# Kernel optimization log

Measured on AMD Instinct MI355X. Metric: run time of the kernel, lower is better.

Reference implementation:

```python
import jax, jax.numpy as jnp
import numpy as np

B, S, T = 4, 512, 512
V, D, F, H, DK, N = 32000, 512, 2048, 8, 64, 6
PAD = 0

# sinusoidal positional encoding table, matching the torch source exactly
_pos = np.arange(max(S, T))[:, None]
_i = np.arange(D // 2)[None, :]
_ang = _pos / (10000.0 ** (2 * _i / D))
_pe = np.empty((max(S, T), D), dtype=np.float32)
_pe[:, 0::2] = np.sin(_ang)
_pe[:, 1::2] = np.cos(_ang)
PE = jnp.asarray(_pe)


def setup_inputs() -> dict:
    key = jax.random.key(0)
    ks = iter(jax.random.split(key, 64))
    s = 0.02
    w = lambda shape: jax.random.normal(next(ks), shape, jnp.float32) * s
    inp = {
        'src': jax.random.randint(next(ks), (B, S), 0, V, jnp.int32),
        'trg': jax.random.randint(next(ks), (B, T), 0, V, jnp.int32),
        'emb_src': w((V, D)).at[PAD].set(0.0),
        'emb_trg': w((V, D)).at[PAD].set(0.0),
        # encoder stacks (leading axis = layer)
        'enc_wq': w((N, D, H * DK)), 'enc_wk': w((N, D, H * DK)),
        'enc_wv': w((N, D, H * DK)), 'enc_wo': w((N, H * DK, D)),
        'enc_ln1_g': jnp.ones((N, D)), 'enc_ln1_b': jnp.zeros((N, D)),
        'enc_w1': w((N, D, F)), 'enc_b1': jnp.zeros((N, F)),
        'enc_w2': w((N, F, D)), 'enc_b2': jnp.zeros((N, D)),
        'enc_ln2_g': jnp.ones((N, D)), 'enc_ln2_b': jnp.zeros((N, D)),
        # decoder stacks
        'dec_wq': w((N, D, H * DK)), 'dec_wk': w((N, D, H * DK)),
        'dec_wv': w((N, D, H * DK)), 'dec_wo': w((N, H * DK, D)),
        'dec_ln1_g': jnp.ones((N, D)), 'dec_ln1_b': jnp.zeros((N, D)),
        'dec_cq': w((N, D, H * DK)), 'dec_ck': w((N, D, H * DK)),
        'dec_cv': w((N, D, H * DK)), 'dec_co': w((N, H * DK, D)),
        'dec_ln2_g': jnp.ones((N, D)), 'dec_ln2_b': jnp.zeros((N, D)),
        'dec_w1': w((N, D, F)), 'dec_b1': jnp.zeros((N, F)),
        'dec_w2': w((N, F, D)), 'dec_b2': jnp.zeros((N, D)),
        'dec_ln3_g': jnp.ones((N, D)), 'dec_ln3_b': jnp.zeros((N, D)),
        'proj': w((D, V)),
    }
    return inp


def _ln(x, g, b, eps=1e-5):
    m = x.mean(-1, keepdims=True)
    v = ((x - m) ** 2).mean(-1, keepdims=True)
    return (x - m) * jax.lax.rsqrt(v + eps) * g + b


def _mha(xq, xkv, wq, wk, wv, wo, mask):
    b, lq, _ = xq.shape
    lk = xkv.shape[1]
    q = (xq @ wq).reshape(b, lq, H, DK).transpose(0, 2, 1, 3)   # bhqd
    k = (xkv @ wk).reshape(b, lk, H, DK).transpose(0, 2, 1, 3)  # bhkd
    v = (xkv @ wv).reshape(b, lk, H, DK).transpose(0, 2, 1, 3)  # bhkd
    scores = jnp.einsum('bhqd,bhkd->bhqk', q, k)
    scores = jnp.where(mask, -jnp.inf, scores)
    attn = jax.nn.softmax(scores * (DK ** -0.5), axis=-1)
    out = jnp.einsum('bhqk,bhkd->bhqd', attn, v)
    out = out.transpose(0, 2, 1, 3).reshape(b, lq, H * DK)
    return out @ wo


def _ffn(x, w1, b1, w2, b2):
    return jax.nn.relu(x @ w1 + b1) @ w2 + b2


def reference(src, trg, emb_src, emb_trg,
              enc_wq, enc_wk, enc_wv, enc_wo, enc_ln1_g, enc_ln1_b,
              enc_w1, enc_b1, enc_w2, enc_b2, enc_ln2_g, enc_ln2_b,
              dec_wq, dec_wk, dec_wv, dec_wo, dec_ln1_g, dec_ln1_b,
              dec_cq, dec_ck, dec_cv, dec_co, dec_ln2_g, dec_ln2_b,
              dec_w1, dec_b1, dec_w2, dec_b2, dec_ln3_g, dec_ln3_b,
              proj):
    scale = D ** 0.5
    src_pad = (src == PAD)[:, None, None, :]                 # [B,1,1,S]
    trg_pad = (trg == PAD)[:, None, None, :]                 # [B,1,1,T]
    causal = jnp.triu(jnp.ones((T, T), bool), 1)[None, None]  # [1,1,T,T]
    trg_mask = trg_pad | causal

    # encoder (dropout = identity in eval)
    x = emb_src[src] * scale + PE[None, :S]

    def enc_step(h, p):
        wq, wk, wv, wo, g1, b1, w1, bb1, w2, bb2, g2, b2 = p
        h = _ln(h + _mha(h, h, wq, wk, wv, wo, src_pad), g1, b1)
        h = _ln(h + _ffn(h, w1, bb1, w2, bb2), g2, b2)
        return h, None

    x_enc, _ = jax.lax.scan(enc_step, x,
        (enc_wq, enc_wk, enc_wv, enc_wo, enc_ln1_g, enc_ln1_b,
         enc_w1, enc_b1, enc_w2, enc_b2, enc_ln2_g, enc_ln2_b))

    # decoder
    y = emb_trg[trg] * scale + PE[None, :T]

    def dec_step(h, p):
        (wq, wk, wv, wo, g1, b1, cq, ck, cv, co, g2, b2,
         w1, bb1, w2, bb2, g3, b3) = p
        h = _ln(h + _mha(h, h, wq, wk, wv, wo, trg_mask), g1, b1)
        h = _ln(h + _mha(h, x_enc, cq, ck, cv, co, src_pad), g2, b2)
        h = _ln(h + _ffn(h, w1, bb1, w2, bb2), g3, b3)
        return h, None

    y, _ = jax.lax.scan(dec_step, y,
        (dec_wq, dec_wk, dec_wv, dec_wo, dec_ln1_g, dec_ln1_b,
         dec_cq, dec_ck, dec_cv, dec_co, dec_ln2_g, dec_ln2_b,
         dec_w1, dec_b1, dec_w2, dec_b2, dec_ln3_g, dec_ln3_b))

    return y @ proj  # [B, T, trg_vocab]
```

## Files before the change

kernel.cpp:

```cpp
#include <hip/hip_runtime.h>
#include <math.h>

#define BBATCH 4
#define SS 512
#define DDIM 512
#define FFN 2048
#define NHEAD 8
#define DHEAD 64
#define NL 6
#define NVOC 32000
#define MTOK (BBATCH*SS)
#define PAD_ID 0
#define MSZE ((size_t)MTOK * DDIM)

typedef unsigned short u16;
typedef __attribute__((ext_vector_type(8))) short short8;
typedef __attribute__((ext_vector_type(4))) float f32x4;

__device__ __forceinline__ u16 f2bf(float f) {
    union { float f; unsigned u; } v; v.f = f;
    unsigned r = ((v.u >> 16) & 1u) + 0x7fffu;
    return (u16)((v.u + r) >> 16);
}

__device__ __forceinline__ void gload16(const u16* g, u16* l) {
    __builtin_amdgcn_global_load_lds(
        (const __attribute__((address_space(1))) void*)g,
        (__attribute__((address_space(3))) void*)l, 16, 0, 0);
}

template<int N> __device__ __forceinline__ void waitv() {
    if constexpr (N == 0)      asm volatile("s_waitcnt vmcnt(0)" ::: "memory");
    else if constexpr (N == 2) asm volatile("s_waitcnt vmcnt(2)" ::: "memory");
    else if constexpr (N == 3) asm volatile("s_waitcnt vmcnt(3)" ::: "memory");
    else if constexpr (N == 4) asm volatile("s_waitcnt vmcnt(4)" ::: "memory");
    else if constexpr (N == 6) asm volatile("s_waitcnt vmcnt(6)" ::: "memory");
    else if constexpr (N == 8) asm volatile("s_waitcnt vmcnt(8)" ::: "memory");
    __builtin_amdgcn_sched_barrier(0);
}
__device__ __forceinline__ void rawbar() {
    __builtin_amdgcn_s_barrier();
    __builtin_amdgcn_sched_barrier(0);
}

template<int BM, int BN, int OUTBF, int RELU, int BIAS>
__device__ __forceinline__ void gemm_core(
    u16* __restrict__ AsB, u16* __restrict__ BsB,
    const u16* __restrict__ A, int lda,
    const u16* __restrict__ B, int ldb,
    void* __restrict__ Cv, int ldc,
    int row0, int col0, int K, const float* __restrict__ bias)
{
    const int tid  = threadIdx.x;
    const int lane = tid & 63;
    const int wid  = tid >> 6;
    const int wr   = wid >> 1, wc = wid & 1;
    constexpr int MF = BM / 32, NF = BN / 32, RA = BM / 64, RB = BN / 64;
    constexpr int LPT = RA + RB;

    const u16* aSrc[RA]; int aOff[RA];
    #pragma unroll
    for (int r = 0; r < RA; r++) {
        int row = (tid >> 2) + r * 64;
        int slot = ((tid & 3) << 4) ^ ((row & 3) << 4);
        aSrc[r] = A + (size_t)(row0 + row) * lda + (slot >> 1);
        aOff[r] = r * 2048 + tid * 8;
    }
    const u16* bSrc[RB]; int bOff[RB];
    #pragma unroll
    for (int r = 0; r < RB; r++) {
        int row = (tid >> 2) + r * 64;
        int slot = ((tid & 3) << 4) ^ ((row & 3) << 4);
        bSrc[r] = B + (size_t)(col0 + row) * ldb + (slot >> 1);
        bOff[r] = r * 2048 + tid * 8;
    }

    f32x4 acc[MF][NF];
    const f32x4 zero = {0.f, 0.f, 0.f, 0.f};
    #pragma unroll
    for (int m = 0; m < MF; m++)
        #pragma unroll
        for (int n = 0; n < NF; n++) acc[m][n] = zero;

    auto issue = [&](int t) {
        u16* ad = AsB + (t & 3) * (BM * 32);
        u16* bd = BsB + (t & 3) * (BN * 32);
        #pragma unroll
        for (int r = 0; r < RA; r++) gload16(aSrc[r] + t * 32, ad + aOff[r]);
        #pragma unroll
        for (int r = 0; r < RB; r++) gload16(bSrc[r] + t * 32, bd + bOff[r]);
    };
    auto comp = [&](int t) {
        const u16* as = AsB + (t & 3) * (BM * 32);
        const u16* bs = BsB + (t & 3) * (BN * 32);
        short8 af[MF], bf[NF];
        #pragma unroll
        for (int m = 0; m < MF; m++) {
            int row = wr * (BM / 2) + m * 16 + (lane & 15);
            int slot = ((lane >> 4) << 4) ^ ((row & 3) << 4);
            af[m] = *(const short8*)&as[row * 32 + (slot >> 1)];
        }
        #pragma unroll
        for (int n = 0; n < NF; n++) {
            int row = wc * (BN / 2) + n * 16 + (lane & 15);
            int slot = ((lane >> 4) << 4) ^ ((row & 3) << 4);
            bf[n] = *(const short8*)&bs[row * 32 + (slot >> 1)];
        }
        __builtin_amdgcn_s_setprio(1);
        #pragma unroll
        for (int m = 0; m < MF; m++)
            #pragma unroll
            for (int n = 0; n < NF; n++)
                acc[m][n] = __builtin_amdgcn_mfma_f32_16x16x32_bf16(af[m], bf[n], acc[m][n], 0, 0, 0);
        __builtin_amdgcn_s_setprio(0);
    };

    const int nt = K / 32;
    issue(0); issue(1); issue(2);
    int t = 0;
    for (; t < nt - 2; ++t) {
        waitv<2 * LPT>();
        rawbar();
        if (t + 3 < nt) issue(t + 3);
        comp(t);
    }
    waitv<LPT>(); rawbar(); comp(nt - 2);
    waitv<0>();   rawbar(); comp(nt - 1);

    const int crow = row0 + wr * (BM / 2);
    const int ccol = col0 + wc * (BN / 2);
    #pragma unroll
    for (int m = 0; m < MF; m++) {
        #pragma unroll
        for (int n = 0; n < NF; n++) {
            int col = ccol + n * 16 + (lane & 15);
            float bv = BIAS ? bias[col] : 0.0f;
            #pragma unroll
            for (int i = 0; i < 4; i++) {
                int row = crow + m * 16 + ((lane >> 4) << 2) + i;
                float v = acc[m][n][i] + bv;
                if (RELU) v = fmaxf(v, 0.0f);
                if (OUTBF) ((u16*)Cv)[(size_t)row * ldc + col] = f2bf(v);
                else       ((float*)Cv)[(size_t)row * ldc + col] = v;
            }
        }
    }
}

template<int BM, int BN, int OUTBF, int RELU, int BIAS, int SWZ = 0>
__global__ __launch_bounds__(256) void mgemm(
    const u16* __restrict__ A, int lda, size_t aSb, size_t aSh,
    const u16* __restrict__ B, int ldb, size_t bSb, size_t bSh,
    void* __restrict__ Cv, int ldc, size_t cSb, size_t cSh,
    int K, const float* __restrict__ bias)
{
    __shared__ __align__(16) u16 As[4 * BM * 32];
    __shared__ __align__(16) u16 Bs[4 * BN * 32];
    int bx = blockIdx.x, by = blockIdx.y;
    if (SWZ) {
        int nwg = gridDim.x * gridDim.y;
        int lin = by * gridDim.x + bx;
        int cpx = nwg >> 3;
        int s = (lin & 7) * cpx + (lin >> 3);
        bx = s % gridDim.x; by = s / gridDim.x;
    }
    const int zb = blockIdx.z >> 3, zh = blockIdx.z & 7;
    const u16* Ab = A + (size_t)zb * aSb + (size_t)zh * aSh;
    const u16* Bb = B + (size_t)zb * bSb + (size_t)zh * bSh;
    void* Cb = OUTBF ? (void*)((u16*)Cv + (size_t)zb * cSb + (size_t)zh * cSh)
                     : (void*)((float*)Cv + (size_t)zb * cSb + (size_t)zh * cSh);
    gemm_core<BM, BN, OUTBF, RELU, BIAS>(As, Bs, Ab, lda, Bb, ldb, Cb, ldc,
                                          by * BM, bx * BN, K, bias);
}

template<int BM, int BN>
__global__ __launch_bounds__(256) void mgemm_dual(
    const u16* __restrict__ A1, int lda1, const u16* __restrict__ B1, int ldb1,
    u16* __restrict__ C1, int ldc1, int nx1, int nblk1,
    const u16* __restrict__ A2, int lda2, const u16* __restrict__ B2, int ldb2,
    u16* __restrict__ C2, int ldc2, int nx2,
    int K)
{
    __shared__ __align__(16) u16 As[4 * BM * 32];
    __shared__ __align__(16) u16 Bs[4 * BN * 32];
    int id = blockIdx.x;
    if (id < nblk1) {
        gemm_core<BM, BN, 1, 0, 0>(As, Bs, A1, lda1, B1, ldb1, C1, ldc1,
                                    (id / nx1) * BM, (id % nx1) * BN, K, nullptr);
    } else {
        id -= nblk1;
        gemm_core<BM, BN, 1, 0, 0>(As, Bs, A2, lda2, B2, ldb2, C2, ldc2,
                                    (id / nx2) * BM, (id % nx2) * BN, K, nullptr);
    }
}

template<int CAUSAL>
__global__ __launch_bounds__(512) void flash_attn(
    const u16* __restrict__ Qp, int ldq,
    const u16* __restrict__ Kp, int ldk,
    const u16* __restrict__ Vtp,
    u16* __restrict__ O,
    const int* __restrict__ ids)
{
    __shared__ __align__(16) u16 Kl[3][64 * 64];
    __shared__ __align__(16) u16 Vl[3][64 * 64];
    __shared__ __align__(16) u16 Pl[8][16 * 64];
    __shared__ float msk[SS];

    const int tid = threadIdx.x, lane = tid & 63, wid = tid >> 6;
    const int bh = blockIdx.y, b = bh >> 3, h = bh & 7;
    const int q0 = blockIdx.x * 128;

    for (int i = tid; i < SS; i += 512)
        msk[i] = (ids[b * SS + i] == PAD_ID) ? -1e30f : 0.0f;

    const int qloc = wid * 16 + (lane & 15);
    const u16* Qb = Qp + (size_t)(b * SS + q0 + qloc) * ldq + h * 64 + ((lane >> 4) * 8);
    short8 qf[2];
    qf[0] = *(const short8*)(Qb);
    qf[1] = *(const short8*)(Qb + 32);

    const u16* Kb = Kp + (size_t)b * SS * ldk + h * 64;
    const u16* Vb = Vtp + (size_t)(h * 64) * MTOK + b * SS;

    auto stage = [&](int buf, int kt) {
        int row = tid >> 3;
        int sl  = tid & 7;
        int ls = sl ^ (row & 7);
        gload16(Kb + (size_t)(kt * 64 + row) * ldk + ls * 8, &Kl[buf][row * 64 + sl * 8]);
        gload16(Vb + (size_t)row * MTOK + kt * 64 + ls * 8, &Vl[buf][row * 64 + sl * 8]);
    };

    const int nt = CAUSAL ? (2 * blockIdx.x + 2) : (SS / 64);

    float m_i[4], l_i[4];
    f32x4 o_acc[4];
    const f32x4 zero = {0.f, 0.f, 0.f, 0.f};
    #pragma unroll
    for (int i = 0; i < 4; i++) { m_i[i] = -1e30f; l_i[i] = 0.0f; }
    #pragma unroll
    for (int n = 0; n < 4; n++) o_acc[n] = zero;

    auto comp = [&](int kt) {
        const int cur = kt % 3;
        f32x4 s_acc[4];
        #pragma unroll
        for (int n = 0; n < 4; n++) s_acc[n] = zero;
        __builtin_amdgcn_s_setprio(1);
        #pragma unroll
        for (int kk = 0; kk < 2; kk++) {
            #pragma unroll
            for (int n = 0; n < 4; n++) {
                int row = n * 16 + (lane & 15);
                int ls = (kk * 4 + (lane >> 4)) ^ (row & 7);
                short8 kf = *(const short8*)&Kl[cur][row * 64 + ls * 8];
                s_acc[n] = __builtin_amdgcn_mfma_f32_16x16x32_bf16(qf[kk], kf, s_acc[n], 0, 0, 0);
            }
        }
        __builtin_amdgcn_s_setprio(0);

        float sv[4][4];
        #pragma unroll
        for (int n = 0; n < 4; n++) {
            int kg = kt * 64 + n * 16 + (lane & 15);
            float mk = msk[kg];
            #pragma unroll
            for (int i = 0; i < 4; i++) {
                float s = s_acc[n][i] * 0.125f + mk;
                if (CAUSAL) {
                    int qg = q0 + wid * 16 + ((lane >> 4) << 2) + i;
                    if (kg > qg) s = -1e30f;
                }
                sv[n][i] = s;
            }
        }
        float pm[4], mn[4], rs[4], ps[4];
        #pragma unroll
        for (int i = 0; i < 4; i++)
            pm[i] = fmaxf(fmaxf(sv[0][i], sv[1][i]), fmaxf(sv[2][i], sv[3][i]));
        #pragma unroll
        for (int i = 0; i < 4; i++) {
            #pragma unroll
            for (int msh = 1; msh <= 8; msh <<= 1)
                pm[i] = fmaxf(pm[i], __shfl_xor(pm[i], msh));
            mn[i] = fmaxf(m_i[i], pm[i]);
            rs[i] = __expf(m_i[i] - mn[i]);
            m_i[i] = mn[i];
        }
        float p[4][4];
        #pragma unroll
        for (int n = 0; n < 4; n++)
            #pragma unroll
            for (int i = 0; i < 4; i++)
                p[n][i] = (sv[n][i] < -1e29f) ? 0.0f : __expf(sv[n][i] - mn[i]);
        #pragma unroll
        for (int i = 0; i < 4; i++) {
            ps[i] = p[0][i] + p[1][i] + p[2][i] + p[3][i];
            #pragma unroll
            for (int msh = 1; msh <= 8; msh <<= 1)
                ps[i] += __shfl_xor(ps[i], msh);
            l_i[i] = l_i[i] * rs[i] + ps[i];
        }
        #pragma unroll
        for (int n = 0; n < 4; n++)
            #pragma unroll
            for (int i = 0; i < 4; i++)
                o_acc[n][i] *= rs[i];

        #pragma unroll
        for (int n = 0; n < 4; n++) {
            int k = n * 16 + (lane & 15);
            #pragma unroll
            for (int i = 0; i < 4; i++) {
                int q = ((lane >> 4) << 2) + i;
                Pl[wid][q * 64 + (((k >> 3) ^ (q & 7)) << 3) + (k & 7)] = f2bf(p[n][i]);
            }
        }
        asm volatile("s_waitcnt lgkmcnt(0)" ::: "memory");
        __builtin_amdgcn_sched_barrier(0);

        __builtin_amdgcn_s_setprio(1);
        #pragma unroll
        for (int kk = 0; kk < 2; kk++) {
            int qrow = lane & 15;
            int lsp = (kk * 4 + (lane >> 4)) ^ (qrow & 7);
            short8 pa = *(const short8*)&Pl[wid][qrow * 64 + lsp * 8];
            #pragma unroll
            for (int nf = 0; nf < 4; nf++) {
                int row = nf * 16 + (lane & 15);
                int vs = (kk * 4 + (lane >> 4)) ^ (row & 7);
                short8 vf = *(const short8*)&Vl[cur][row * 64 + vs * 8];
                o_acc[nf] = __builtin_amdgcn_mfma_f32_16x16x32_bf16(pa, vf, o_acc[nf], 0, 0, 0);
            }
        }
        __builtin_amdgcn_s_setprio(0);
    };

    stage(0, 0);
    stage(1, 1);
    int t = 0;
    for (; t < nt - 1; ++t) {
        waitv<2>();
        rawbar();
        if (t + 2 < nt) stage((t + 2) % 3, t + 2);
        comp(t);
    }
    waitv<0>(); rawbar(); comp(nt - 1);

    #pragma unroll
    for (int nf = 0; nf < 4; nf++) {
        int d = h * 64 + nf * 16 + (lane & 15);
        #pragma unroll
        for (int i = 0; i < 4; i++) {
            int qg = b * SS + q0 + wid * 16 + ((lane >> 4) << 2) + i;
            O[(size_t)qg * DDIM + d] = f2bf(o_acc[nf][i] / l_i[i]);
        }
    }
}

__device__ __forceinline__ void transp_core(const float* __restrict__ src, u16* __restrict__ dst,
                                            int N, int K, int n0, int k0)
{
    __shared__ u16 t[64][65];
    const int tid = threadIdx.x;
    #pragma unroll
    for (int i = 0; i < 16; i++) {
        int idx = tid + i * 256;
        int kr = idx >> 6, nc = idx & 63;
        t[kr][nc] = f2bf(src[(size_t)(k0 + kr) * N + n0 + nc]);
    }
    __syncthreads();
    #pragma unroll
    for (int i = 0; i < 16; i++) {
        int idx = tid + i * 256;
        int nr = idx >> 6, kc = idx & 63;
        dst[(size_t)(n0 + nr) * K + k0 + kc] = t[kc][nr];
    }
}

__global__ __launch_bounds__(256) void transp(const float* __restrict__ src, u16* __restrict__ dst,
                                              int N, int K, size_t sStride, size_t dStride)
{
    transp_core(src + (size_t)blockIdx.z * sStride, dst + (size_t)blockIdx.z * dStride,
                N, K, blockIdx.x * 64, blockIdx.y * 64);
}

#define OFF_QK 0u
#define OFF_WV 524288u
#define OFF_WO 786432u
#define OFF_CQ 1048576u
#define OFF_CK 1310720u
#define OFF_CV 1572864u
#define OFF_CO 1835008u
#define OFF_W1 2097152u
#define OFF_W2 3145728u
#define WBLK   4194304u
#define M2CNT  262144u
#define MF1CNT 1048576u

__global__ __launch_bounds__(256) void transpW(
    const float* p0, const float* p1, const float* p2, const float* p3,
    const float* p4, const float* p5, const float* p6, const float* p7,
    const float* p8, const float* p9, const float* p10, const float* p11,
    u16* __restrict__ wreg)
{
    int z = blockIdx.z;
    int w = z % 12, l = z / 12;
    const float* ptrs[12] = {p0,p1,p2,p3,p4,p5,p6,p7,p8,p9,p10,p11};
    const float* src = ptrs[w] + (size_t)l * M2CNT;
    u16* dst = wreg + (w < 4 ? (size_t)l * WBLK + (size_t)w * M2CNT
                             : (size_t)(NL + l) * WBLK + (size_t)(w - 4) * M2CNT);
    transp_core(src, dst, 512, 512, blockIdx.x * 64, blockIdx.y * 64);
}

__global__ __launch_bounds__(256) void transpF1(const float* __restrict__ e,
                                                const float* __restrict__ d, u16* __restrict__ wreg)
{
    int z = blockIdx.z; int l = z % NL, w = z / NL;
    const float* src = (w ? d : e) + (size_t)l * MF1CNT;
    u16* dst = wreg + (size_t)(w * NL + l) * WBLK + OFF_W1;
    transp_core(src, dst, 2048, 512, blockIdx.x * 64, blockIdx.y * 64);
}

__global__ __launch_bounds__(256) void transpF2(const float* __restrict__ e,
                                                const float* __restrict__ d, u16* __restrict__ wreg)
{
    int z = blockIdx.z; int l = z % NL, w = z / NL;
    const float* src = (w ? d : e) + (size_t)l * MF1CNT;
    u16* dst = wreg + (size_t)(w * NL + l) * WBLK + OFF_W2;
    transp_core(src, dst, 512, 2048, blockIdx.x * 64, blockIdx.y * 64);
}

__global__ void pe_kernel(float* __restrict__ PEt)
{
    int pos = blockIdx.x, d = threadIdx.x;
    int i = d >> 1;
    double freq = exp(-(2.0 * (double)i / (double)DDIM) * log(10000.0));
    double ang = (double)pos * freq;
    PEt[pos * DDIM + d] = (float)((d & 1) ? cos(ang) : sin(ang));
}

__global__ void embed_kernel(const int* __restrict__ src, const int* __restrict__ trg,
                             const float* __restrict__ es, const float* __restrict__ et,
                             const float* __restrict__ PEt,
                             float* __restrict__ X, u16* __restrict__ Xb,
                             float* __restrict__ Y, u16* __restrict__ Ybf)
{
    int gtok = blockIdx.x;
    int d = threadIdx.x;
    bool dec = gtok >= MTOK;
    int tok = dec ? gtok - MTOK : gtok;
    int pos = tok & (SS - 1);
    int id = (dec ? trg : src)[tok];
    const float* emb = dec ? et : es;
    float val = emb[(size_t)id * DDIM + d] * 22.62741699796952f + PEt[pos * DDIM + d];
    (dec ? Y : X)[(size_t)tok * DDIM + d] = val;
    (dec ? Ybf : Xb)[(size_t)tok * DDIM + d] = f2bf(val);
}

__global__ __launch_bounds__(256) void add_ln_kernel(float* __restrict__ x,
    const float* __restrict__ addv, const float* __restrict__ g,
    const float* __restrict__ bta, u16* __restrict__ xb)
{
    int row = blockIdx.x;
    int tid = threadIdx.x;
    size_t base = (size_t)row * DDIM;
    __shared__ float sbuf[4];

    float v0 = x[base + tid]       + addv[base + tid];
    float v1 = x[base + tid + 256] + addv[base + tid + 256];

    float s = v0 + v1;
    #pragma unroll
    for (int o = 32; o > 0; o >>= 1) s += __shfl_down(s, o);
    if ((tid & 63) == 0) sbuf[tid >> 6] = s;
    __syncthreads();
    float mean = (sbuf[0] + sbuf[1] + sbuf[2] + sbuf[3]) * (1.0f / DDIM);
    __syncthreads();

    float d0 = v0 - mean, d1 = v1 - mean;
    float ss = d0 * d0 + d1 * d1;
    #pragma unroll
    for (int o = 32; o > 0; o >>= 1) ss += __shfl_down(ss, o);
    if ((tid & 63) == 0) sbuf[tid >> 6] = ss;
    __syncthreads();
    float var = (sbuf[0] + sbuf[1] + sbuf[2] + sbuf[3]) * (1.0f / DDIM);
    float inv = rsqrtf(var + 1e-5f);

    float o0 = d0 * inv * g[tid]       + bta[tid];
    float o1 = d1 * inv * g[tid + 256] + bta[tid + 256];
    x[base + tid] = o0;
    x[base + tid + 256] = o1;
    xb[base + tid] = f2bf(o0);
    xb[base + tid + 256] = f2bf(o1);
}

__global__ __launch_bounds__(256) void add_ln_red(float* __restrict__ x,
    const float* __restrict__ part, const float* __restrict__ bias,
    const float* __restrict__ g, const float* __restrict__ bta, u16* __restrict__ xb)
{
    int row = blockIdx.x;
    int tid = threadIdx.x;
    size_t base = (size_t)row * DDIM;
    __shared__ float sbuf[4];

    float v0 = x[base + tid]       + bias[tid];
    float v1 = x[base + tid + 256] + bias[tid + 256];
    #pragma unroll
    for (int s4 = 0; s4 < 4; s4++) {
        v0 += part[s4 * MSZE + base + tid];
        v1 += part[s4 * MSZE + base + tid + 256];
    }

    float s = v0 + v1;
    #pragma unroll
    for (int o = 32; o > 0; o >>= 1) s += __shfl_down(s, o);
    if ((tid & 63) == 0) sbuf[tid >> 6] = s;
    __syncthreads();
    float mean = (sbuf[0] + sbuf[1] + sbuf[2] + sbuf[3]) * (1.0f / DDIM);
    __syncthreads();

    float d0 = v0 - mean, d1 = v1 - mean;
    float ss = d0 * d0 + d1 * d1;
    #pragma unroll
    for (int o = 32; o > 0; o >>= 1) ss += __shfl_down(ss, o);
    if ((tid & 63) == 0) sbuf[tid >> 6] = ss;
    __syncthreads();
    float var = (sbuf[0] + sbuf[1] + sbuf[2] + sbuf[3]) * (1.0f / DDIM);
    float inv = rsqrtf(var + 1e-5f);

    float o0 = d0 * inv * g[tid]       + bta[tid];
    float o1 = d1 * inv * g[tid + 256] + bta[tid + 256];
    x[base + tid] = o0;
    x[base + tid + 256] = o1;
    xb[base + tid] = f2bf(o0);
    xb[base + tid + 256] = f2bf(o1);
}

extern "C" void kernel_launch(void* const* d_in, const int* in_sizes, int n_in,
                              void* d_out, int out_size, void* d_ws, size_t ws_size,
                              hipStream_t stream)
{
    (void)in_sizes; (void)n_in; (void)out_size;

    const int*   src      = (const int*)  d_in[0];
    const int*   trg      = (const int*)  d_in[1];
    const float* emb_src  = (const float*)d_in[2];
    const float* emb_trg  = (const float*)d_in[3];
    const float* enc_wq   = (const float*)d_in[4];
    const float* enc_wk   = (const float*)d_in[5];
    const float* enc_wv   = (const float*)d_in[6];
    const float* enc_wo   = (const float*)d_in[7];
    const float* enc_ln1g = (const float*)d_in[8];
    const float* enc_ln1b = (const float*)d_in[9];
    const float* enc_w1   = (const float*)d_in[10];
    const float* enc_b1   = (const float*)d_in[11];
    const float* enc_w2   = (const float*)d_in[12];
    const float* enc_b2   = (const float*)d_in[13];
    const float* enc_ln2g = (const float*)d_in[14];
    const float* enc_ln2b = (const float*)d_in[15];
    const float* dec_wq   = (const float*)d_in[16];
    const float* dec_wk   = (const float*)d_in[17];
    const float* dec_wv   = (const float*)d_in[18];
    const float* dec_wo   = (const float*)d_in[19];
    const float* dec_ln1g = (const float*)d_in[20];
    const float* dec_ln1b = (const float*)d_in[21];
    const float* dec_cq   = (const float*)d_in[22];
    const float* dec_ck   = (const float*)d_in[23];
    const float* dec_cv   = (const float*)d_in[24];
    const float* dec_co   = (const float*)d_in[25];
    const float* dec_ln2g = (const float*)d_in[26];
    const float* dec_ln2b = (const float*)d_in[27];
    const float* dec_w1   = (const float*)d_in[28];
    const float* dec_b1   = (const float*)d_in[29];
    const float* dec_w2   = (const float*)d_in[30];
    const float* dec_b2   = (const float*)d_in[31];
    const float* dec_ln3g = (const float*)d_in[32];
    const float* dec_ln3b = (const float*)d_in[33];
    const float* proj     = (const float*)d_in[34];

    float* OUT = (float*)d_out;
    char* base = (char*)d_ws;

    size_t off = 0;
    auto carve = [&](size_t bytes) { char* p = base + off; off += (bytes + 255) & ~(size_t)255; return p; };

    float* X      = (float*)carve(MSZE * 4);
    float* Yb     = (float*)carve(MSZE * 4);
    float* T1     = (float*)carve(MSZE * 4);
    u16*   Xb     = (u16*)  carve(MSZE * 2);
    u16*   Ybf    = (u16*)  carve(MSZE * 2);
    u16*   QKb    = (u16*)  carve((size_t)MTOK * 1024 * 2);
    u16*   Vt     = (u16*)  carve((size_t)512 * MTOK * 2);
    u16*   CTX    = (u16*)  carve(MSZE * 2);
    u16*   HFF    = (u16*)  carve((size_t)MTOK * FFN * 2);
    u16*   Kcr    = (u16*)  carve((size_t)NL * MTOK * 512 * 2);
    u16*   Vtc    = (u16*)  carve((size_t)NL * 512 * MTOK * 2);
    u16*   projT  = (u16*)  carve((size_t)NVOC * 512 * 2);
    float* PEt    = (float*)carve((size_t)SS * DDIM * 4);
    float* Tp4    = (float*)carve((size_t)4 * MSZE * 4);

    const size_t WFULL_B = (size_t)12 * WBLK * 2;
    bool full = (ws_size >= off + WFULL_B);
    u16* Wreg = (u16*)carve(full ? WFULL_B : (size_t)WBLK * 2);

    auto T = [&](const float* s, u16* d, int Kd, int Nd, size_t ss, size_t ds, int L) {
        transp<<<dim3(Nd / 64, Kd / 64, L), 256, 0, stream>>>(s, d, Nd, Kd, ss, ds);
    };

    pe_kernel<<<SS, DDIM, 0, stream>>>(PEt);
    T(proj, projT, 512, NVOC, 0, 0, 1);
    if (full) {
        transpW<<<dim3(8, 8, 12 * NL), 256, 0, stream>>>(
            enc_wq, enc_wk, enc_wv, enc_wo,
            dec_wq, dec_wk, dec_wv, dec_wo,
            dec_cq, dec_ck, dec_cv, dec_co, Wreg);
        transpF1<<<dim3(32, 8, 2 * NL), 256, 0, stream>>>(enc_w1, dec_w1, Wreg);
        transpF2<<<dim3(8, 32, 2 * NL), 256, 0, stream>>>(enc_w2, dec_w2, Wreg);
    }
    embed_kernel<<<2 * MTOK, DDIM, 0, stream>>>(src, trg, emb_src, emb_trg, PEt, X, Xb, Yb, Ybf);

    auto self_attn = [&](const u16* xsrc, const u16* wb, const int* mask_ids, int causal) {
        mgemm_dual<128, 128><<<dim3(192), 256, 0, stream>>>(
            xsrc, 512, wb + OFF_QK, 512, QKb, 1024, 8, 128,
            wb + OFF_WV, 512, xsrc, 512, Vt, MTOK, 16,
            512);
        if (causal)
            flash_attn<1><<<dim3(4, 32), 512, 0, stream>>>(QKb, 1024, QKb + 512, 1024, Vt, CTX, mask_ids);
        else
            flash_attn<0><<<dim3(4, 32), 512, 0, stream>>>(QKb, 1024, QKb + 512, 1024, Vt, CTX, mask_ids);
        mgemm<64, 64, 0, 0, 0><<<dim3(8, 32, 1), 256, 0, stream>>>(
            CTX, 512, 0, 0, wb + OFF_WO, 512, 0, 0, T1, 512, 0, 0, 512, nullptr);
    };

    auto ffn = [&](const u16* xsrc, const u16* wb, const float* b1) {
        mgemm<128, 128, 1, 1, 1><<<dim3(16, 16, 1), 256, 0, stream>>>(
            xsrc, 512, 0, 0, wb + OFF_W1, 512, 0, 0, HFF, FFN, 0, 0, 512, b1);
        mgemm<128, 128, 0, 0, 0><<<dim3(4, 16, 4), 256, 0, stream>>>(
            HFF, 2048, 0, 512, wb + OFF_W2, 2048, 0, 512,
            Tp4, 512, 0, MSZE, 512, nullptr);
    };

    const size_t M2 = M2CNT, MF1 = MF1CNT;

    for (int l = 0; l < NL; l++) {
        u16* wb;
        if (full) wb = Wreg + (size_t)l * WBLK;
        else {
            wb = Wreg;
            T(enc_wq + l * M2,  wb + OFF_QK,          512, 512,  0, 0, 1);
            T(enc_wk + l * M2,  wb + OFF_QK + M2,     512, 512,  0, 0, 1);
            T(enc_wv + l * M2,  wb + OFF_WV,          512, 512,  0, 0, 1);
            T(enc_wo + l * M2,  wb + OFF_WO,          512, 512,  0, 0, 1);
            T(enc_w1 + l * MF1, wb + OFF_W1,          512, 2048, 0, 0, 1);
            T(enc_w2 + l * MF1, wb + OFF_W2,          2048, 512, 0, 0, 1);
        }
        self_attn(Xb, wb, src, 0);
        add_ln_kernel<<<MTOK, 256, 0, stream>>>(X, T1, enc_ln1g + l * DDIM, enc_ln1b + l * DDIM, Xb);
        ffn(Xb, wb, enc_b1 + l * FFN);
        add_ln_red<<<MTOK, 256, 0, stream>>>(X, Tp4, enc_b2 + l * DDIM,
                                             enc_ln2g + l * DDIM, enc_ln2b + l * DDIM, Xb);
    }

    if (full) {
        u16* Wd = Wreg + (size_t)NL * WBLK;
        mgemm<128, 128, 1, 0, 0><<<dim3(4, 16, NL), 256, 0, stream>>>(
            Xb, 512, 0, 0, Wd + OFF_CK, 512, 0, WBLK, Kcr, 512, 0, (size_t)MTOK * 512, 512, nullptr);
        mgemm<128, 128, 1, 0, 0><<<dim3(16, 4, NL), 256, 0, stream>>>(
            Wd + OFF_CV, 512, 0, WBLK, Xb, 512, 0, 0, Vtc, MTOK, 0, (size_t)512 * MTOK, 512, nullptr);
    }

    for (int l = 0; l < NL; l++) {
        u16* wb;
        if (full) wb = Wreg + (size_t)(NL + l) * WBLK;
        else {
            wb = Wreg;
            T(dec_wq + l * M2,  wb + OFF_QK,          512, 512,  0, 0, 1);
            T(dec_wk + l * M2,  wb + OFF_QK + M2,     512, 512,  0, 0, 1);
            T(dec_wv + l * M2,  wb + OFF_WV,          512, 512,  0, 0, 1);
            T(dec_wo + l * M2,  wb + OFF_WO,          512, 512,  0, 0, 1);
            T(dec_cq + l * M2,  wb + OFF_CQ,          512, 512,  0, 0, 1);
            T(dec_ck + l * M2,  wb + OFF_CK,          512, 512,  0, 0, 1);
            T(dec_cv + l * M2,  wb + OFF_CV,          512, 512,  0, 0, 1);
            T(dec_co + l * M2,  wb + OFF_CO,          512, 512,  0, 0, 1);
            T(dec_w1 + l * MF1, wb + OFF_W1,          512, 2048, 0, 0, 1);
            T(dec_w2 + l * MF1, wb + OFF_W2,          2048, 512, 0, 0, 1);
            mgemm<128, 128, 1, 0, 0><<<dim3(4, 16, 1), 256, 0, stream>>>(
                Xb, 512, 0, 0, wb + OFF_CK, 512, 0, 0, Kcr + (size_t)l * MTOK * 512, 512, 0, 0, 512, nullptr);
            mgemm<128, 128, 1, 0, 0><<<dim3(16, 4, 1), 256, 0, stream>>>(
                wb + OFF_CV, 512, 0, 0, Xb, 512, 0, 0, Vtc + (size_t)l * 512 * MTOK, MTOK, 0, 0, 512, nullptr);
        }
        self_attn(Ybf, wb, trg, 1);
        add_ln_kernel<<<MTOK, 256, 0, stream>>>(Yb, T1, dec_ln1g + l * DDIM, dec_ln1b + l * DDIM, Ybf);
        mgemm<64, 64, 1, 0, 0><<<dim3(8, 32, 1), 256, 0, stream>>>(
            Ybf, 512, 0, 0, wb + OFF_CQ, 512, 0, 0, QKb, 1024, 0, 0, 512, nullptr);
        flash_attn<0><<<dim3(4, 32), 512, 0, stream>>>(
            QKb, 1024, Kcr + (size_t)l * MTOK * 512, 512, Vtc + (size_t)l * 512 * MTOK, CTX, src);
        mgemm<64, 64, 0, 0, 0><<<dim3(8, 32, 1), 256, 0, stream>>>(
            CTX, 512, 0, 0, wb + OFF_CO, 512, 0, 0, T1, 512, 0, 0, 512, nullptr);
        add_ln_kernel<<<MTOK, 256, 0, stream>>>(Yb, T1, dec_ln2g + l * DDIM, dec_ln2b + l * DDIM, Ybf);
        ffn(Ybf, wb, dec_b1 + l * FFN);
        add_ln_red<<<MTOK, 256, 0, stream>>>(Yb, Tp4, dec_b2 + l * DDIM,
                                             dec_ln3g + l * DDIM, dec_ln3b + l * DDIM, Ybf);
    }

    mgemm<128, 128, 0, 0, 0, 1><<<dim3(NVOC / 128, 16, 1), 256, 0, stream>>>(
        Ybf, 512, 0, 0, projT, 512, 0, 0, OUT, NVOC, 0, 0, 512, nullptr);
}
```

Before: 1.547 ms.

## Fuse output-projection and FFN-down GEMMs with residual add and LayerNorm

Adds a gemm_ln kernel in which each block computes a full 128x512 output row tile, adds bias and the residual, and applies LayerNorm in the epilogue. This replaces the Wo/W2 GEMMs, the split-K partial buffer and the separate add+LN kernels, removing intermediate global traffic and launches. Positional encoding is now computed inline in the embedding kernel instead of from a precomputed table. The fused kernel launches only 16 blocks, so most compute units sit idle and parallelism drops sharply compared with the earlier 256-block grids.

```diff
diff --git a/kernel.cpp b/kernel.cpp
--- a/kernel.cpp
+++ b/kernel.cpp
@@ -30,12 +30,14 @@
 }
 
 template<int N> __device__ __forceinline__ void waitv() {
-    if constexpr (N == 0)      asm volatile("s_waitcnt vmcnt(0)" ::: "memory");
-    else if constexpr (N == 2) asm volatile("s_waitcnt vmcnt(2)" ::: "memory");
-    else if constexpr (N == 3) asm volatile("s_waitcnt vmcnt(3)" ::: "memory");
-    else if constexpr (N == 4) asm volatile("s_waitcnt vmcnt(4)" ::: "memory");
-    else if constexpr (N == 6) asm volatile("s_waitcnt vmcnt(6)" ::: "memory");
-    else if constexpr (N == 8) asm volatile("s_waitcnt vmcnt(8)" ::: "memory");
+    if constexpr (N == 0)       asm volatile("s_waitcnt vmcnt(0)" ::: "memory");
+    else if constexpr (N == 2)  asm volatile("s_waitcnt vmcnt(2)" ::: "memory");
+    else if constexpr (N == 3)  asm volatile("s_waitcnt vmcnt(3)" ::: "memory");
+    else if constexpr (N == 4)  asm volatile("s_waitcnt vmcnt(4)" ::: "memory");
+    else if constexpr (N == 5)  asm volatile("s_waitcnt vmcnt(5)" ::: "memory");
+    else if constexpr (N == 6)  asm volatile("s_waitcnt vmcnt(6)" ::: "memory");
+    else if constexpr (N == 8)  asm volatile("s_waitcnt vmcnt(8)" ::: "memory");
+    else if constexpr (N == 10) asm volatile("s_waitcnt vmcnt(10)" ::: "memory");
     __builtin_amdgcn_sched_barrier(0);
 }
 __device__ __forceinline__ void rawbar() {
@@ -191,6 +193,142 @@
         id -= nblk1;
         gemm_core<BM, BN, 1, 0, 0>(As, Bs, A2, lda2, B2, ldb2, C2, ldc2,
                                     (id / nx2) * BM, (id % nx2) * BN, K, nullptr);
+    }
+}
+
+template<int BIAS>
+__global__ __launch_bounds__(512) void gemm_ln(
+    const u16* __restrict__ A, int lda,
+    const u16* __restrict__ Bw,
+    const float* __restrict__ bias,
+    const float* __restrict__ g, const float* __restrict__ bta,
+    float* __restrict__ X, u16* __restrict__ Xb,
+    int K)
+{
+    __shared__ __align__(16) u16 As[3 * 128 * 32];
+    __shared__ __align__(16) u16 Bs[3 * 512 * 32];
+    __shared__ float red[128][8];
+    __shared__ float red2[128][2];
+
+    const int tid = threadIdx.x, lane = tid & 63, wid = tid >> 6;
+    const int wr = wid >> 2, wc = wid & 3;
+    const int row0 = blockIdx.x * 128;
+    const int l15 = lane & 15, l4 = lane >> 4;
+
+    const int arow = tid >> 2;
+    const int aseg = (tid & 3) ^ (arow & 3);
+    const u16* aSrc = A + (size_t)(row0 + arow) * lda + aseg * 8;
+    const u16* bSrc[4];
+    #pragma unroll
+    for (int r = 0; r < 4; r++) {
+        int brow = (tid >> 2) + r * 128;
+        int bseg = (tid & 3) ^ (brow & 3);
+        bSrc[r] = Bw + (size_t)brow * K + bseg * 8;
+    }
+
+    f32x4 acc[4][8];
+    const f32x4 zero = {0.f, 0.f, 0.f, 0.f};
+    #pragma unroll
+    for (int m = 0; m < 4; m++)
+        #pragma unroll
+        for (int n = 0; n < 8; n++) acc[m][n] = zero;
+
+    auto issue = [&](int t) {
+        u16* ad = As + (t % 3) * 4096;
+        u16* bd = Bs + (t % 3) * 16384;
+        gload16(aSrc + t * 32, ad + tid * 8);
+        #pragma unroll
+        for (int r = 0; r < 4; r++) gload16(bSrc[r] + t * 32, bd + r * 4096 + tid * 8);
+    };
+    auto comp = [&](int t) {
+        const u16* as = As + (t % 3) * 4096;
+        const u16* bs = Bs + (t % 3) * 16384;
+        short8 af[4], bf[8];
+        #pragma unroll
+        for (int m = 0; m < 4; m++) {
+            int row = wr * 64 + m * 16 + l15;
+            int chunk = (l4 ^ (row & 3)) * 8;
+            af[m] = *(const short8*)&as[row * 32 + chunk];
+        }
+        #pragma unroll
+        for (int n = 0; n < 8; n++) {
+            int brow = wc * 128 + n * 16 + l15;
+            int chunk = (l4 ^ (brow & 3)) * 8;
+            bf[n] = *(const short8*)&bs[brow * 32 + chunk];
+        }
+        __builtin_amdgcn_s_setprio(1);
+        #pragma unroll
+        for (int m = 0; m < 4; m++)
+            #pragma unroll
+            for (int n = 0; n < 8; n++)
+                acc[m][n] = __builtin_amdgcn_mfma_f32_16x16x32_bf16(af[m], bf[n], acc[m][n], 0, 0, 0);
+        __builtin_amdgcn_s_setprio(0);
+    };
+
+    const int nt = K / 32;
+    issue(0); issue(1);
+    for (int t = 0; t < nt - 1; ++t) {
+        waitv<5>();
+        rawbar();
+        if (t + 2 < nt) issue(t + 2);
+        comp(t);
+    }
+    waitv<0>(); rawbar(); comp(nt - 1);
+
+    #pragma unroll
+    for (int n = 0; n < 8; n++) {
+        int col = wc * 128 + n * 16 + l15;
+        float bv = BIAS ? bias[col] : 0.0f;
+        #pragma unroll
+        for (int m = 0; m < 4; m++)
+            #pragma unroll
+            for (int i = 0; i < 4; i++) {
+                int row = row0 + wr * 64 + m * 16 + l4 * 4 + i;
+                acc[m][n][i] += bv + X[(size_t)row * DDIM + col];
+            }
+    }
+    #pragma unroll
+    for (int m = 0; m < 4; m++)
+        #pragma unroll
+        for (int i = 0; i < 4; i++) {
+            float s = 0.f, q = 0.f;
+            #pragma unroll
+            for (int n = 0; n < 8; n++) { float v = acc[m][n][i]; s += v; q += v * v; }
+            #pragma unroll
+            for (int msk = 1; msk <= 8; msk <<= 1) {
+                s += __shfl_xor(s, msk);
+                q += __shfl_xor(q, msk);
+            }
+            if (l15 == 0) {
+                int rl = wr * 64 + m * 16 + l4 * 4 + i;
+                red[rl][wc * 2]     = s;
+                red[rl][wc * 2 + 1] = q;
+            }
+        }
+    __syncthreads();
+    if (tid < 128) {
+        float s = red[tid][0] + red[tid][2] + red[tid][4] + red[tid][6];
+        float q = red[tid][1] + red[tid][3] + red[tid][5] + red[tid][7];
+        float mean = s * (1.0f / DDIM);
+        float var  = q * (1.0f / DDIM) - mean * mean;
+        red2[tid][0] = mean;
+        red2[tid][1] = rsqrtf(var + 1e-5f);
+    }
+    __syncthreads();
+    #pragma unroll
+    for (int n = 0; n < 8; n++) {
+        int col = wc * 128 + n * 16 + l15;
+        float gv = g[col], b2 = bta[col];
+        #pragma unroll
+        for (int m = 0; m < 4; m++)
+            #pragma unroll
+            for (int i = 0; i < 4; i++) {
+                int rl = wr * 64 + m * 16 + l4 * 4 + i;
+                float o = (acc[m][n][i] - red2[rl][0]) * red2[rl][1] * gv + b2;
+                size_t idx = (size_t)(row0 + rl) * DDIM + col;
+                X[idx] = o;
+                Xb[idx] = f2bf(o);
+            }
     }
 }
 
@@ -431,18 +569,8 @@
     transp_core(src, dst, 512, 2048, blockIdx.x * 64, blockIdx.y * 64);
 }
 
-__global__ void pe_kernel(float* __restrict__ PEt)
-{
-    int pos = blockIdx.x, d = threadIdx.x;
-    int i = d >> 1;
-    double freq = exp(-(2.0 * (double)i / (double)DDIM) * log(10000.0));
-    double ang = (double)pos * freq;
-    PEt[pos * DDIM + d] = (float)((d & 1) ? cos(ang) : sin(ang));
-}
-
 __global__ void embed_kernel(const int* __restrict__ src, const int* __restrict__ trg,
                              const float* __restrict__ es, const float* __restrict__ et,
-                             const float* __restrict__ PEt,
                              float* __restrict__ X, u16* __restrict__ Xb,
                              float* __restrict__ Y, u16* __restrict__ Ybf)
 {
@@ -453,88 +581,13 @@
     int pos = tok & (SS - 1);
     int id = (dec ? trg : src)[tok];
     const float* emb = dec ? et : es;
-    float val = emb[(size_t)id * DDIM + d] * 22.62741699796952f + PEt[pos * DDIM + d];
+    int i = d >> 1;
+    double freq = exp(-(2.0 * (double)i / (double)DDIM) * log(10000.0));
+    double ang = (double)pos * freq;
+    float pe = (float)((d & 1) ? cos(ang) : sin(ang));
+    float val = emb[(size_t)id * DDIM + d] * 22.62741699796952f + pe;
     (dec ? Y : X)[(size_t)tok * DDIM + d] = val;
     (dec ? Ybf : Xb)[(size_t)tok * DDIM + d] = f2bf(val);
-}
-
-__global__ __launch_bounds__(256) void add_ln_kernel(float* __restrict__ x,
-    const float* __restrict__ addv, const float* __restrict__ g,
-    const float* __restrict__ bta, u16* __restrict__ xb)
-{
-    int row = blockIdx.x;
-    int tid = threadIdx.x;
-    size_t base = (size_t)row * DDIM;
-    __shared__ float sbuf[4];
-
-    float v0 = x[base + tid]       + addv[base + tid];
-    float v1 = x[base + tid + 256] + addv[base + tid + 256];
-
-    float s = v0 + v1;
-    #pragma unroll
-    for (int o = 32; o > 0; o >>= 1) s += __shfl_down(s, o);
-    if ((tid & 63) == 0) sbuf[tid >> 6] = s;
-    __syncthreads();
-    float mean = (sbuf[0] + sbuf[1] + sbuf[2] + sbuf[3]) * (1.0f / DDIM);
-    __syncthreads();
-
-    float d0 = v0 - mean, d1 = v1 - mean;
-    float ss = d0 * d0 + d1 * d1;
-    #pragma unroll
-    for (int o = 32; o > 0; o >>= 1) ss += __shfl_down(ss, o);
-    if ((tid & 63) == 0) sbuf[tid >> 6] = ss;
-    __syncthreads();
-    float var = (sbuf[0] + sbuf[1] + sbuf[2] + sbuf[3]) * (1.0f / DDIM);
-    float inv = rsqrtf(var + 1e-5f);
-
-    float o0 = d0 * inv * g[tid]       + bta[tid];
-    float o1 = d1 * inv * g[tid + 256] + bta[tid + 256];
-    x[base + tid] = o0;
-    x[base + tid + 256] = o1;
-    xb[base + tid] = f2bf(o0);
-    xb[base + tid + 256] = f2bf(o1);
-}
-
-__global__ __launch_bounds__(256) void add_ln_red(float* __restrict__ x,
-    const float* __restrict__ part, const float* __restrict__ bias,
-    const float* __restrict__ g, const float* __restrict__ bta, u16* __restrict__ xb)
-{
-    int row = blockIdx.x;
-    int tid = threadIdx.x;
-    size_t base = (size_t)row * DDIM;
-    __shared__ float sbuf[4];
-
-    float v0 = x[base + tid]       + bias[tid];
-    float v1 = x[base + tid + 256] + bias[tid + 256];
-    #pragma unroll
-    for (int s4 = 0; s4 < 4; s4++) {
-        v0 += part[s4 * MSZE + base + tid];
-        v1 += part[s4 * MSZE + base + tid + 256];
-    }
-
-    float s = v0 + v1;
-    #pragma unroll
-    for (int o = 32; o > 0; o >>= 1) s += __shfl_down(s, o);
-    if ((tid & 63) == 0) sbuf[tid >> 6] = s;
-    __syncthreads();
-    float mean = (sbuf[0] + sbuf[1] + sbuf[2] + sbuf[3]) * (1.0f / DDIM);
-    __syncthreads();
-
-    float d0 = v0 - mean, d1 = v1 - mean;
-    float ss = d0 * d0 + d1 * d1;
-    #pragma unroll
-    for (int o = 32; o > 0; o >>= 1) ss += __shfl_down(ss, o);
-    if ((tid & 63) == 0) sbuf[tid >> 6] = ss;
-    __syncthreads();
-    float var = (sbuf[0] + sbuf[1] + sbuf[2] + sbuf[3]) * (1.0f / DDIM);
-    float inv = rsqrtf(var + 1e-5f);
-
-    float o0 = d0 * inv * g[tid]       + bta[tid];
-    float o1 = d1 * inv * g[tid + 256] + bta[tid + 256];
-    x[base + tid] = o0;
-    x[base + tid + 256] = o1;
-    xb[base + tid] = f2bf(o0);
-    xb[base + tid + 256] = f2bf(o1);
 }
 
 extern "C" void kernel_launch(void* const* d_in, const int* in_sizes, int n_in,
@@ -587,7 +640,6 @@
 
     float* X      = (float*)carve(MSZE * 4);
     float* Yb     = (float*)carve(MSZE * 4);
-    float* T1     = (float*)carve(MSZE * 4);
     u16*   Xb     = (u16*)  carve(MSZE * 2);
     u16*   Ybf    = (u16*)  carve(MSZE * 2);
     u16*   QKb    = (u16*)  carve((size_t)MTOK * 1024 * 2);
@@ -597,8 +649,6 @@
     u16*   Kcr    = (u16*)  carve((size_t)NL * MTOK * 512 * 2);
     u16*   Vtc    = (u16*)  carve((size_t)NL * 512 * MTOK * 2);
     u16*   projT  = (u16*)  carve((size_t)NVOC * 512 * 2);
-    float* PEt    = (float*)carve((size_t)SS * DDIM * 4);
-    float* Tp4    = (float*)carve((size_t)4 * MSZE * 4);
 
     const size_t WFULL_B = (size_t)12 * WBLK * 2;
     bool full = (ws_size >= off + WFULL_B);
@@ -608,7 +658,6 @@
         transp<<<dim3(Nd / 64, Kd / 64, L), 256, 0, stream>>>(s, d, Nd, Kd, ss, ds);
     };
 
-    pe_kernel<<<SS, DDIM, 0, stream>>>(PEt);
     T(proj, projT, 512, NVOC, 0, 0, 1);
     if (full) {
         transpW<<<dim3(8, 8, 12 * NL), 256, 0, stream>>>(
@@ -618,7 +667,7 @@
         transpF1<<<dim3(32, 8, 2 * NL), 256, 0, stream>>>(enc_w1, dec_w1, Wreg);
         transpF2<<<dim3(8, 32, 2 * NL), 256, 0, stream>>>(enc_w2, dec_w2, Wreg);
     }
-    embed_kernel<<<2 * MTOK, DDIM, 0, stream>>>(src, trg, emb_src, emb_trg, PEt, X, Xb, Yb, Ybf);
+    embed_kernel<<<2 * MTOK, DDIM, 0, stream>>>(src, trg, emb_src, emb_trg, X, Xb, Yb, Ybf);
 
     auto self_attn = [&](const u16* xsrc, const u16* wb, const int* mask_ids, int causal) {
         mgemm_dual<128, 128><<<dim3(192), 256, 0, stream>>>(
@@ -629,16 +678,6 @@
             flash_attn<1><<<dim3(4, 32), 512, 0, stream>>>(QKb, 1024, QKb + 512, 1024, Vt, CTX, mask_ids);
         else
             flash_attn<0><<<dim3(4, 32), 512, 0, stream>>>(QKb, 1024, QKb + 512, 1024, Vt, CTX, mask_ids);
-        mgemm<64, 64, 0, 0, 0><<<dim3(8, 32, 1), 256, 0, stream>>>(
-            CTX, 512, 0, 0, wb + OFF_WO, 512, 0, 0, T1, 512, 0, 0, 512, nullptr);
-    };
-
-    auto ffn = [&](const u16* xsrc, const u16* wb, const float* b1) {
-        mgemm<128, 128, 1, 1, 1><<<dim3(16, 16, 1), 256, 0, stream>>>(
-            xsrc, 512, 0, 0, wb + OFF_W1, 512, 0, 0, HFF, FFN, 0, 0, 512, b1);
-        mgemm<128, 128, 0, 0, 0><<<dim3(4, 16, 4), 256, 0, stream>>>(
-            HFF, 2048, 0, 512, wb + OFF_W2, 2048, 0, 512,
-            Tp4, 512, 0, MSZE, 512, nullptr);
     };
 
     const size_t M2 = M2CNT, MF1 = MF1CNT;
@@ -656,10 +695,12 @@
             T(enc_w2 + l * MF1, wb + OFF_W2,          2048, 512, 0, 0, 1);
         }
         self_attn(Xb, wb, src, 0);
-        add_ln_kernel<<<MTOK, 256, 0, stream>>>(X, T1, enc_ln1g + l * DDIM, enc_ln1b + l * DDIM, Xb);
-        ffn(Xb, wb, enc_b1 + l * FFN);
-        add_ln_red<<<MTOK, 256, 0, stream>>>(X, Tp4, enc_b2 + l * DDIM,
-                                             enc_ln2g + l * DDIM, enc_ln2b + l * DDIM, Xb);
+        gemm_ln<0><<<16, 512, 0, stream>>>(CTX, 512, wb + OFF_WO, nullptr,
+            enc_ln1g + l * DDIM, enc_ln1b + l * DDIM, X, Xb, 512);
+        mgemm<128, 128, 1, 1, 1><<<dim3(16, 16, 1), 256, 0, stream>>>(
+            Xb, 512, 0, 0, wb + OFF_W1, 512, 0, 0, HFF, FFN, 0, 0, 512, enc_b1 + l * FFN);
+        gemm_ln<1><<<16, 512, 0, stream>>>(HFF, 2048, wb + OFF_W2, enc_b2 + l * DDIM,
+            enc_ln2g + l * DDIM, enc_ln2b + l * DDIM, X, Xb, 2048);
     }
 
     if (full) {
@@ -691,17 +732,18 @@
                 wb + OFF_CV, 512, 0, 0, Xb, 512, 0, 0, Vtc + (size_t)l * 512 * MTOK, MTOK, 0, 0, 512, nullptr);
         }
         self_attn(Ybf, wb, trg, 1);
-        add_ln_kernel<<<MTOK, 256, 0, stream>>>(Yb, T1, dec_ln1g + l * DDIM, dec_ln1b + l * DDIM, Ybf);
+        gemm_ln<0><<<16, 512, 0, stream>>>(CTX, 512, wb + OFF_WO, nullptr,
+            dec_ln1g + l * DDIM, dec_ln1b + l * DDIM, Yb, Ybf, 512);
         mgemm<64, 64, 1, 0, 0><<<dim3(8, 32, 1), 256, 0, stream>>>(
             Ybf, 512, 0, 0, wb + OFF_CQ, 512, 0, 0, QKb, 1024, 0, 0, 512, nullptr);
         flash_attn<0><<<dim3(4, 32), 512, 0, stream>>>(
             QKb, 1024, Kcr + (size_t)l * MTOK * 512, 512, Vtc + (size_t)l * 512 * MTOK, CTX, src);
-        mgemm<64, 64, 0, 0, 0><<<dim3(8, 32, 1), 256, 0, stream>>>(
-            CTX, 512, 0, 0, wb + OFF_CO, 512, 0, 0, T1, 512, 0, 0, 512, nullptr);
-        add_ln_kernel<<<MTOK, 256, 0, stream>>>(Yb, T1, dec_ln2g + l * DDIM, dec_ln2b + l * DDIM, Ybf);
-        ffn(Ybf, wb, dec_b1 + l * FFN);
-        add_ln_red<<<MTOK, 256, 0, stream>>>(Yb, Tp4, dec_b2 + l * DDIM,
-                                             dec_ln3g + l * DDIM, dec_ln3b + l * DDIM, Ybf);
+        gemm_ln<0><<<16, 512, 0, stream>>>(CTX, 512, wb + OFF_CO, nullptr,
+            dec_ln2g + l * DDIM, dec_ln2b + l * DDIM, Yb, Ybf, 512);
+        mgemm<128, 128, 1, 1, 1><<<dim3(16, 16, 1), 256, 0, stream>>>(
+            Ybf, 512, 0, 0, wb + OFF_W1, 512, 0, 0, HFF, FFN, 0, 0, 512, dec_b1 + l * FFN);
+        gemm_ln<1><<<16, 512, 0, stream>>>(HFF, 2048, wb + OFF_W2, dec_b2 + l * DDIM,
+            dec_ln3g + l * DDIM, dec_ln3b + l * DDIM, Yb, Ybf, 2048);
     }
 
     mgemm<128, 128, 0, 0, 0, 1><<<dim3(NVOC / 128, 16, 1), 256, 0, stream>>>(
```

Result: slower. 3.607 ms (+133.1%).
